# Performance work log

Hardware: AMD Instinct MI355X
Metric: run time of the kernel (lower is better)

The kernel has to match this reference:

```python
import jax, jax.numpy as jnp
import numpy as np

D_MODEL = 1024
N_HEADS = 16
D_HEAD = D_MODEL // N_HEADS
RANK = 128
KNOW_RANK = 128
N_COMPRESS = 64
N_EXPAND = 32
N_KNOW = 16384
TOPK_C = 8
TOPK_E = 4
KNOW_K = 8
B, S = 8, 1024
EPS_LN = 1e-5


def setup_inputs() -> dict:
    key = jax.random.key(0)
    ks = jax.random.split(key, 16)
    inp = {
        'x': jax.random.normal(ks[0], (B, S, D_MODEL), jnp.float32),
        'importance': jax.random.uniform(ks[1], (B, S), jnp.float32),
        # routers, stored as [d_model, n] so out = x @ W
        'Wc': jax.random.normal(ks[2], (D_MODEL, N_COMPRESS), jnp.float32) * 0.02,
        'WQr': jax.random.normal(ks[3], (D_MODEL, N_EXPAND), jnp.float32) * 0.02,
        'WKr': jax.random.normal(ks[4], (D_MODEL, N_EXPAND), jnp.float32) * 0.02,
        'WVr': jax.random.normal(ks[5], (D_MODEL, N_EXPAND), jnp.float32) * 0.02,
        'Wm': jax.random.normal(ks[6], (D_MODEL, N_COMPRESS), jnp.float32) * 0.02,
        # shared neuron pools
        'compress_neurons': jax.random.normal(ks[7], (N_COMPRESS, D_MODEL, RANK), jnp.float32) / np.sqrt(D_MODEL),
        'expand_pool': jax.random.normal(ks[8], (N_EXPAND, RANK, D_MODEL), jnp.float32) / np.sqrt(RANK),
        'knowledge_K': jax.random.normal(ks[9], (N_KNOW, KNOW_RANK), jnp.float32) * 0.02,
        'knowledge_V': jax.random.normal(ks[10], (N_KNOW, D_MODEL), jnp.float32) * 0.02,
        # output projection stored as [d_in, d_out]
        'W_O': jax.random.normal(ks[11], (D_MODEL, D_MODEL), jnp.float32) / np.sqrt(D_MODEL),
        'ln1_s': jnp.ones((D_MODEL,), jnp.float32),
        'ln1_b': jnp.zeros((D_MODEL,), jnp.float32),
        'ln2_s': jnp.ones((D_MODEL,), jnp.float32),
        'ln2_b': jnp.zeros((D_MODEL,), jnp.float32),
    }
    return inp


def _layernorm(x, s, b):
    mu = jnp.mean(x, axis=-1, keepdims=True)
    var = jnp.mean(jnp.square(x - mu), axis=-1, keepdims=True)
    return (x - mu) * jax.lax.rsqrt(var + EPS_LN) * s + b


def _topk_sparsify(w, k):
    # w: [B, n] -> sparse renormalized weights [B, n]
    vals, idx = jax.lax.top_k(w, k)
    rows = jnp.arange(w.shape[0])[:, None]
    sparse = jnp.zeros_like(w).at[rows, idx].set(vals)
    return sparse / (jnp.sum(sparse, axis=-1, keepdims=True) + 1e-8)


def _route(nx, importance, W, k):
    pref = jax.nn.softmax(jnp.einsum('bsd,dn->bsn', nx, W), axis=-1)
    dense = jnp.einsum('bs,bsn->bn', importance, pref)
    return _topk_sparsify(dense, k)


def _forward(x, importance, Wc, WQr, WKr, WVr, Wm, compress_neurons,
             expand_pool, knowledge_K, knowledge_V, W_O, ln1_s, ln1_b, ln2_s, ln2_b):
    Bx, Sx, D = x.shape
    n1 = _layernorm(x, ln1_s, ln1_b)

    # --- attention routing ---
    cw = _route(n1, importance, Wc, TOPK_C)
    ewQ = _route(n1, importance, WQr, TOPK_E)
    ewK = _route(n1, importance, WKr, TOPK_E)
    ewV = _route(n1, importance, WVr, TOPK_E)

    # --- synthesized low-rank attention weights ---
    shared_compress = jnp.einsum('bn,ndr->bdr', cw, compress_neurons)
    h = jnp.einsum('bsd,bdr->bsr', n1, shared_compress)
    EQ = jnp.einsum('bn,nrd->brd', ewQ, expand_pool)
    EK = jnp.einsum('bn,nrd->brd', ewK, expand_pool)
    EV = jnp.einsum('bn,nrd->brd', ewV, expand_pool)
    Q = jnp.einsum('bsr,brd->bsd', h, EQ).reshape(Bx, Sx, N_HEADS, D_HEAD).transpose(0, 2, 1, 3)
    K = jnp.einsum('bsr,brd->bsd', h, EK).reshape(Bx, Sx, N_HEADS, D_HEAD).transpose(0, 2, 1, 3)
    V = jnp.einsum('bsr,brd->bsd', h, EV).reshape(Bx, Sx, N_HEADS, D_HEAD).transpose(0, 2, 1, 3)

    scores = jnp.einsum('bhqd,bhkd->bhqk', Q, K) / np.sqrt(D_HEAD)
    causal = jnp.tril(jnp.ones((Sx, Sx), bool))
    scores = jnp.where(causal, scores, jnp.finfo(scores.dtype).min)
    attn = jax.nn.softmax(scores, axis=-1)
    attn_out = jnp.einsum('bhqk,bhkd->bhqd', attn, V).transpose(0, 2, 1, 3).reshape(Bx, Sx, D)
    attn_out = attn_out @ W_O
    x = x + attn_out

    # --- memory ---
    n2 = _layernorm(x, ln2_s, ln2_b)
    mw = _route(n2, importance, Wm, TOPK_C)
    sc_m = jnp.einsum('bn,ndr->bdr', mw, compress_neurons)
    Qm = jnp.einsum('bsd,bdr->bsr', n2, sc_m)  # knowledge_rank == rank -> no query_proj
    mscores = jnp.einsum('bsr,nr->bsn', Qm, knowledge_K) / np.sqrt(KNOW_RANK)
    topv, topi = jax.lax.top_k(mscores, KNOW_K)
    w = jax.nn.softmax(topv, axis=-1)  # [B,S,k]
    selV = knowledge_V[topi]  # [B,S,k,D]
    mem_out = jnp.einsum('bsk,bskd->bsd', w, selV)
    return x + mem_out


def reference(x, importance, Wc, WQr, WKr, WVr, Wm, compress_neurons,
              expand_pool, knowledge_K, knowledge_V, W_O, ln1_s, ln1_b, ln2_s, ln2_b):
    return _forward(x, importance, Wc, WQr, WKr, WVr, Wm, compress_neurons,
                    expand_pool, knowledge_K, knowledge_V, W_O, ln1_s, ln1_b, ln2_s, ln2_b)
```

## Files before the change

### kernel.cpp

```cpp
#include <hip/hip_runtime.h>
#include <hip/hip_bf16.h>

#define BD 8
#define SD 1024
#define DM 1024
#define NH 16
#define DH 64
#define RK 128
#define NK 16384

typedef __attribute__((ext_vector_type(8))) short bf16x8;
typedef __attribute__((ext_vector_type(4))) float f32x4;

__device__ __forceinline__ unsigned short f2b(float f) {
    unsigned u = __float_as_uint(f);
    unsigned r = (u + 0x7FFFu + ((u >> 16) & 1u)) >> 16;
    return (unsigned short)r;
}
__device__ __forceinline__ float b2f(unsigned short h) {
    return __uint_as_float(((unsigned)h) << 16);
}

__global__ void __launch_bounds__(256) ln_kernel(const float* __restrict__ x,
                                                 const float* __restrict__ sc,
                                                 const float* __restrict__ bi,
                                                 unsigned short* __restrict__ outh,
                                                 unsigned short* __restrict__ outl) {
    const int tok = blockIdx.x;
    __shared__ float xs[DM];
    __shared__ float red[256];
    const float* xp = x + (size_t)tok * DM;
    float s = 0.f;
    for (int i = threadIdx.x; i < DM; i += 256) { float v = xp[i]; xs[i] = v; s += v; }
    red[threadIdx.x] = s; __syncthreads();
    for (int st = 128; st; st >>= 1) { if (threadIdx.x < st) red[threadIdx.x] += red[threadIdx.x + st]; __syncthreads(); }
    float mu = red[0] * (1.f / DM);
    __syncthreads();
    float vs = 0.f;
    for (int i = threadIdx.x; i < DM; i += 256) { float d = xs[i] - mu; vs += d * d; }
    red[threadIdx.x] = vs; __syncthreads();
    for (int st = 128; st; st >>= 1) { if (threadIdx.x < st) red[threadIdx.x] += red[threadIdx.x + st]; __syncthreads(); }
    float rs = rsqrtf(red[0] * (1.f / DM) + 1e-5f);
    for (int i = threadIdx.x; i < DM; i += 256) {
        float v = (xs[i] - mu) * rs * sc[i] + bi[i];
        unsigned short h = f2b(v);
        outh[(size_t)tok * DM + i] = h;
        outl[(size_t)tok * DM + i] = f2b(v - b2f(h));
    }
}

__global__ void __launch_bounds__(256) prep_kernel(const float* __restrict__ Wc,
                                                   const float* __restrict__ WQr,
                                                   const float* __restrict__ WKr,
                                                   const float* __restrict__ WVr,
                                                   const float* __restrict__ Wm,
                                                   unsigned short* __restrict__ WTh,
                                                   unsigned short* __restrict__ WTl,
                                                   const float* __restrict__ WO,
                                                   unsigned short* __restrict__ WOt,
                                                   const float* __restrict__ kK,
                                                   unsigned short* __restrict__ kKb) {
    __shared__ float ls[64][65];
    const int t = threadIdx.x;
    const int bid = blockIdx.x;
    if (bid < 1024) {
        const int i = bid * 256 + t;
        const int c = i >> 10, d = i & 1023;
        float v = 0.f;
        if (c < 64)       v = Wc[d * 64 + c];
        else if (c < 96)  v = WQr[d * 32 + c - 64];
        else if (c < 128) v = WKr[d * 32 + c - 96];
        else if (c < 160) v = WVr[d * 32 + c - 128];
        else if (c >= 192) v = Wm[d * 64 + c - 192];
        unsigned short h = f2b(v);
        WTh[i] = h;
        WTl[i] = f2b(v - b2f(h));
    } else if (bid < 1280) {
        const int bz = bid - 1024;
        const int r0 = (bz >> 4) * 64, c0 = (bz & 15) * 64;
        #pragma unroll
        for (int p = 0; p < 16; p++) {
            const int e = p * 256 + t;
            const int r = e >> 6, c = e & 63;
            ls[r][c] = WO[(size_t)(r0 + r) * DM + c0 + c];
        }
        __syncthreads();
        #pragma unroll
        for (int p = 0; p < 16; p++) {
            const int e = p * 256 + t;
            const int c = e >> 6, r = e & 63;
            WOt[(size_t)(c0 + c) * DM + r0 + r] = f2b(ls[r][c]);
        }
    } else {
        const int i = (bid - 1280) * 256 + t;
        const float scale = 0.0883883476483184f;
        float4 v = ((const float4*)kK)[i];
        unsigned r0 = (unsigned)f2b(v.x * scale) | ((unsigned)f2b(v.y * scale) << 16);
        unsigned r1 = (unsigned)f2b(v.z * scale) | ((unsigned)f2b(v.w * scale) << 16);
        uint2 o; o.x = r0; o.y = r1;
        ((uint2*)kKb)[i] = o;
    }
}

__global__ void __launch_bounds__(256) gemm_split(const unsigned short* __restrict__ Ah,
                                                  const unsigned short* __restrict__ Al,
                                                  const unsigned short* __restrict__ Bh,
                                                  const unsigned short* __restrict__ Bl,
                                                  float* __restrict__ C,
                                                  int N, int K) {
    const int row0 = blockIdx.y * 64, col0 = blockIdx.x * 64;
    const int t = threadIdx.x;
    const int w = t >> 6, l = t & 63, lq = l & 15, lg = l >> 4;
    __shared__ unsigned short sAh[64 * 64];
    __shared__ unsigned short sAl[64 * 64];
    __shared__ unsigned short sBh[64 * 64];
    __shared__ unsigned short sBl[64 * 64];
    f32x4 acc[4];
    #pragma unroll
    for (int ni = 0; ni < 4; ni++) acc[ni] = f32x4{0.f, 0.f, 0.f, 0.f};

    for (int k0 = 0; k0 < K; k0 += 64) {
        __syncthreads();
        #pragma unroll
        for (int p = 0; p < 2; p++) {
            const int e = t * 8 + p * 2048;
            const int row = e >> 6, col = e & 63;
            const int sw = (e * 2) ^ ((row & 7) << 4);
            *(bf16x8*)((char*)sAh + sw) = *(const bf16x8*)(Ah + (size_t)(row0 + row) * K + k0 + col);
            *(bf16x8*)((char*)sAl + sw) = *(const bf16x8*)(Al + (size_t)(row0 + row) * K + k0 + col);
            *(bf16x8*)((char*)sBh + sw) = *(const bf16x8*)(Bh + (size_t)(col0 + row) * K + k0 + col);
            *(bf16x8*)((char*)sBl + sw) = *(const bf16x8*)(Bl + (size_t)(col0 + row) * K + k0 + col);
        }
        __syncthreads();
        #pragma unroll
        for (int kk = 0; kk < 2; kk++) {
            bf16x8 ah, al, bh[4], bl[4];
            {
                const int r = w * 16 + lq;
                const int off = (r * 128 + lg * 16 + kk * 64) ^ ((r & 7) << 4);
                ah = *(const bf16x8*)((const char*)sAh + off);
                al = *(const bf16x8*)((const char*)sAl + off);
            }
            #pragma unroll
            for (int ni = 0; ni < 4; ni++) {
                const int r = ni * 16 + lq;
                const int off = (r * 128 + lg * 16 + kk * 64) ^ ((r & 7) << 4);
                bh[ni] = *(const bf16x8*)((const char*)sBh + off);
                bl[ni] = *(const bf16x8*)((const char*)sBl + off);
            }
            #pragma unroll
            for (int ni = 0; ni < 4; ni++) {
                acc[ni] = __builtin_amdgcn_mfma_f32_16x16x32_bf16(ah, bh[ni], acc[ni], 0, 0, 0);
                acc[ni] = __builtin_amdgcn_mfma_f32_16x16x32_bf16(ah, bl[ni], acc[ni], 0, 0, 0);
                acc[ni] = __builtin_amdgcn_mfma_f32_16x16x32_bf16(al, bh[ni], acc[ni], 0, 0, 0);
            }
        }
    }
    #pragma unroll
    for (int j = 0; j < 4; j++) {
        const int row = row0 + w * 16 + lg * 4 + j;
        #pragma unroll
        for (int ni = 0; ni < 4; ni++)
            C[(size_t)row * N + col0 + ni * 16 + lq] = acc[ni][j];
    }
}

__global__ void __launch_bounds__(256) gemm_split_sm2(const unsigned short* __restrict__ Ah,
                                                      const unsigned short* __restrict__ Al,
                                                      const unsigned short* __restrict__ Bh,
                                                      const unsigned short* __restrict__ Bl,
                                                      const float* __restrict__ imp,
                                                      float* __restrict__ partial) {
    const int row0 = blockIdx.x * 64;
    const int K = DM;
    const int t = threadIdx.x;
    const int w = t >> 6, l = t & 63, lq = l & 15, lg = l >> 4;
    __shared__ unsigned short sAh[64 * 64];
    __shared__ unsigned short sAl[64 * 64];
    __shared__ unsigned short sBh[64 * 64];
    __shared__ unsigned short sBl[64 * 64];
    __shared__ float wsm[64][65];
    f32x4 acc[4];
    #pragma unroll
    for (int ni = 0; ni < 4; ni++) acc[ni] = f32x4{0.f, 0.f, 0.f, 0.f};

    for (int k0 = 0; k0 < K; k0 += 64) {
        __syncthreads();
        #pragma unroll
        for (int p = 0; p < 2; p++) {
            const int e = t * 8 + p * 2048;
            const int row = e >> 6, col = e & 63;
            const int sw = (e * 2) ^ ((row & 7) << 4);
            *(bf16x8*)((char*)sAh + sw) = *(const bf16x8*)(Ah + (size_t)(row0 + row) * K + k0 + col);
            *(bf16x8*)((char*)sAl + sw) = *(const bf16x8*)(Al + (size_t)(row0 + row) * K + k0 + col);
            *(bf16x8*)((char*)sBh + sw) = *(const bf16x8*)(Bh + (size_t)(row) * K + k0 + col);
            *(bf16x8*)((char*)sBl + sw) = *(const bf16x8*)(Bl + (size_t)(row) * K + k0 + col);
        }
        __syncthreads();
        #pragma unroll
        for (int kk = 0; kk < 2; kk++) {
            bf16x8 ah, al, bh[4], bl[4];
            {
                const int r = w * 16 + lq;
                const int off = (r * 128 + lg * 16 + kk * 64) ^ ((r & 7) << 4);
                ah = *(const bf16x8*)((const char*)sAh + off);
                al = *(const bf16x8*)((const char*)sAl + off);
            }
            #pragma unroll
            for (int ni = 0; ni < 4; ni++) {
                const int r = ni * 16 + lq;
                const int off = (r * 128 + lg * 16 + kk * 64) ^ ((r & 7) << 4);
                bh[ni] = *(const bf16x8*)((const char*)sBh + off);
                bl[ni] = *(const bf16x8*)((const char*)sBl + off);
            }
            #pragma unroll
            for (int ni = 0; ni < 4; ni++) {
                acc[ni] = __builtin_amdgcn_mfma_f32_16x16x32_bf16(ah, bh[ni], acc[ni], 0, 0, 0);
                acc[ni] = __builtin_amdgcn_mfma_f32_16x16x32_bf16(ah, bl[ni], acc[ni], 0, 0, 0);
                acc[ni] = __builtin_amdgcn_mfma_f32_16x16x32_bf16(al, bh[ni], acc[ni], 0, 0, 0);
            }
        }
    }
    #pragma unroll
    for (int j = 0; j < 4; j++) {
        float mx = fmaxf(fmaxf(acc[0][j], acc[1][j]), fmaxf(acc[2][j], acc[3][j]));
        #pragma unroll
        for (int d = 1; d < 16; d <<= 1) mx = fmaxf(mx, __shfl_xor(mx, d));
        float e0 = __expf(acc[0][j] - mx), e1 = __expf(acc[1][j] - mx);
        float e2 = __expf(acc[2][j] - mx), e3 = __expf(acc[3][j] - mx);
        float ss = e0 + e1 + e2 + e3;
        #pragma unroll
        for (int d = 1; d < 16; d <<= 1) ss += __shfl_xor(ss, d);
        const int rl = w * 16 + lg * 4 + j;
        const float scl = imp[row0 + rl] / ss;
        wsm[rl][lq]      = e0 * scl;
        wsm[rl][16 + lq] = e1 * scl;
        wsm[rl][32 + lq] = e2 * scl;
        wsm[rl][48 + lq] = e3 * scl;
    }
    __syncthreads();
    if (t < 64) {
        float s = 0.f;
        for (int k = 0; k < 64; k++) s += wsm[k][t];
        const int b = row0 >> 10, chunk = (row0 >> 6) & 15;
        partial[((size_t)(b * 16 + chunk)) * 224 + 160 + t] = s;
    }
}

__global__ void __launch_bounds__(256) softpref_red(const float* __restrict__ lgt,
                                                    const float* __restrict__ imp,
                                                    float* __restrict__ partial) {
    const int b = blockIdx.x, chunk = blockIdx.y;
    __shared__ float wp[64][161];
    const int t = threadIdx.x;
    const int tl = t >> 2, sg = t & 3;
    const int tok = b * SD + chunk * 64 + tl;
    const int o = (sg == 0) ? 0 : (64 + 32 * (sg - 1));
    const int n = (sg == 0) ? 64 : 32;
    const float* lp = lgt + (size_t)tok * 192 + o;
    float m = -1e30f;
    for (int i = 0; i < n; i++) m = fmaxf(m, lp[i]);
    float ss = 0.f;
    for (int i = 0; i < n; i++) ss += __expf(lp[i] - m);
    const float scl = imp[tok] / ss;
    for (int i = 0; i < n; i++) wp[tl][o + i] = __expf(lp[i] - m) * scl;
    __syncthreads();
    if (t < 160) {
        float s = 0.f;
        for (int k = 0; k < 64; k++) s += wp[k][t];
        partial[((size_t)(b * 16 + chunk)) * 224 + t] = s;
    }
}

__global__ void topk_kernel(const float* __restrict__ partial,
                            int* __restrict__ ridx, float* __restrict__ rw,
                            int r0, int nr) {
    __shared__ float dv[40][65];
    const int t = threadIdx.x;
    if (t >= BD * nr) return;
    const int b = t / nr, r = r0 + (t % nr);
    const int offs[5] = {0, 64, 96, 128, 160};
    const int ns[5]   = {64, 32, 32, 32, 64};
    const int ks[5]   = {8, 4, 4, 4, 8};
    const int n = ns[r], k = ks[r], off = offs[r];
    for (int i = 0; i < n; i++) {
        float s = 0.f;
        for (int c = 0; c < 16; c++) s += partial[((size_t)(b * 16 + c)) * 224 + off + i];
        dv[t][i] = s;
    }
    unsigned long long mask = 0;
    float vals[8]; int idxs[8];
    float ssum = 0.f;
    for (int kk = 0; kk < k; kk++) {
        float best = -1e30f; int bi = 0;
        for (int i = 0; i < n; i++)
            if (!((mask >> i) & 1ull) && dv[t][i] > best) { best = dv[t][i]; bi = i; }
        mask |= 1ull << bi;
        vals[kk] = best; idxs[kk] = bi; ssum += best;
    }
    float inv = 1.f / (ssum + 1e-8f);
    for (int kk = 0; kk < 8; kk++) {
        ridx[(b * 5 + r) * 8 + kk] = (kk < k) ? idxs[kk] : 0;
        rw[(b * 5 + r) * 8 + kk]   = (kk < k) ? vals[kk] * inv : 0.f;
    }
}

__global__ void __launch_bounds__(256) combine_all_kernel(const float* __restrict__ cneu,
                                                          const float* __restrict__ epool,
                                                          const int* __restrict__ ridx,
                                                          const float* __restrict__ rw,
                                                          unsigned short* __restrict__ scompT,
                                                          unsigned short* __restrict__ E3t) {
    __shared__ float ls[64][65];
    const int t = threadIdx.x;
    const int bid = blockIdx.x;
    const float* pool;
    int b, router, r0, c0, Rp, Cp;
    unsigned short* op;
    if (bid < 256) {
        b = bid >> 5;
        const int rem = bid & 31;
        c0 = (rem & 1) * 64; r0 = (rem >> 1) * 64;
        Rp = DM; Cp = RK; router = 0; pool = cneu;
        op = scompT + (size_t)b * DM * RK;
    } else {
        const int e = bid - 256;
        const int z = e >> 5;
        const int rem = e & 31;
        c0 = (rem & 15) * 64; r0 = (rem >> 4) * 64;
        b = z & 7; router = 1 + (z >> 3);
        Rp = RK; Cp = DM; pool = epool;
        op = E3t + (size_t)b * 3 * DM * RK + (size_t)(router - 1) * DM * RK;
    }
    const int* ii = ridx + (b * 5 + router) * 8;
    const float* ww = rw + (b * 5 + router) * 8;
    const int kc = (router == 0) ? 8 : 4;
    const int rr = t >> 4, cc = (t & 15) * 4;
    #pragma unroll
    for (int p = 0; p < 4; p++) {
        const int r = rr + p * 16;
        float4 acc = {0.f, 0.f, 0.f, 0.f};
        for (int kk = 0; kk < kc; kk++) {
            const float w = ww[kk];
            float4 v = *(const float4*)&pool[((size_t)ii[kk] * Rp + r0 + r) * Cp + c0 + cc];
            acc.x += w * v.x; acc.y += w * v.y; acc.z += w * v.z; acc.w += w * v.w;
        }
        ls[r][cc] = acc.x; ls[r][cc + 1] = acc.y; ls[r][cc + 2] = acc.z; ls[r][cc + 3] = acc.w;
    }
    __syncthreads();
    #pragma unroll
    for (int q = 0; q < 2; q++) {
        const int c = (t >> 3) + q * 32;
        const int r8 = (t & 7) * 8;
        union { unsigned short s[8]; bf16x8 v; } u;
        #pragma unroll
        for (int j = 0; j < 8; j++) u.s[j] = f2b(ls[r8 + j][c]);
        *(bf16x8*)(op + (size_t)(c0 + c) * Rp + r0 + r8) = u.v;
    }
}

__global__ void __launch_bounds__(256) combine_t_kernel(const float* __restrict__ pool,
                                                        const int* __restrict__ ridx,
                                                        const float* __restrict__ rw,
                                                        int router, int kc,
                                                        unsigned short* __restrict__ outT,
                                                        int Rp, int Cp, long long sOut) {
    const int b = blockIdx.z;
    const int r0 = blockIdx.y * 64, c0 = blockIdx.x * 64;
    __shared__ float ls[64][65];
    const int* ii = ridx + (b * 5 + router) * 8;
    const float* ww = rw + (b * 5 + router) * 8;
    const int t = threadIdx.x;
    const int rr = t >> 4, cc = (t & 15) * 4;
    #pragma unroll
    for (int p = 0; p < 4; p++) {
        const int r = rr + p * 16;
        float4 acc = {0.f, 0.f, 0.f, 0.f};
        for (int kk = 0; kk < kc; kk++) {
            const float w = ww[kk];
            float4 v = *(const float4*)&pool[((size_t)ii[kk] * Rp + r0 + r) * Cp + c0 + cc];
            acc.x += w * v.x; acc.y += w * v.y; acc.z += w * v.z; acc.w += w * v.w;
        }
        ls[r][cc] = acc.x; ls[r][cc + 1] = acc.y; ls[r][cc + 2] = acc.z; ls[r][cc + 3] = acc.w;
    }
    __syncthreads();
    unsigned short* op = outT + (size_t)b * sOut;
    #pragma unroll
    for (int q = 0; q < 2; q++) {
        const int c = (t >> 3) + q * 32;
        const int r8 = (t & 7) * 8;
        union { unsigned short s[8]; bf16x8 v; } u;
        #pragma unroll
        for (int j = 0; j < 8; j++) u.s[j] = f2b(ls[r8 + j][c]);
        *(bf16x8*)(op + (size_t)(c0 + c) * Rp + r0 + r8) = u.v;
    }
}

template<int OUTB, int HASX>
__global__ void __launch_bounds__(256) gemm_bf16(const unsigned short* __restrict__ A,
                                                 const unsigned short* __restrict__ Bt,
                                                 const float* __restrict__ X,
                                                 void* __restrict__ Cv,
                                                 int M, int N, int K,
                                                 long long sA, long long sB, long long sC) {
    const int bz = blockIdx.z;
    const unsigned short* Ab = A + (size_t)bz * sA;
    const unsigned short* Btb = Bt + (size_t)bz * sB;
    const int row0 = blockIdx.y * 128, col0 = blockIdx.x * 128;
    const int t = threadIdx.x;
    const int w = t >> 6, l = t & 63, lq = l & 15, lg = l >> 4;
    const int wr = w >> 1, wc = w & 1;
    __shared__ unsigned short As[128 * 64];
    __shared__ unsigned short Bs[128 * 64];
    f32x4 acc[4][4];
    #pragma unroll
    for (int mi = 0; mi < 4; mi++)
        #pragma unroll
        for (int ni = 0; ni < 4; ni++) acc[mi][ni] = f32x4{0.f, 0.f, 0.f, 0.f};

    for (int k0 = 0; k0 < K; k0 += 64) {
        __syncthreads();
        #pragma unroll
        for (int p = 0; p < 4; p++) {
            const int e = t * 8 + p * 2048;
            const int row = e >> 6, col = e & 63;
            bf16x8 va = *(const bf16x8*)(Ab + (size_t)(row0 + row) * K + k0 + col);
            *(bf16x8*)((char*)As + ((row * 128 + col * 2) ^ ((row & 7) << 4))) = va;
            bf16x8 vb = *(const bf16x8*)(Btb + (size_t)(col0 + row) * K + k0 + col);
            *(bf16x8*)((char*)Bs + ((row * 128 + col * 2) ^ ((row & 7) << 4))) = vb;
        }
        __syncthreads();
        #pragma unroll
        for (int kk = 0; kk < 2; kk++) {
            bf16x8 af[4], bg[4];
            #pragma unroll
            for (int mi = 0; mi < 4; mi++) {
                const int r = wr * 64 + mi * 16 + lq;
                af[mi] = *(const bf16x8*)((const char*)As + ((r * 128 + lg * 16 + kk * 64) ^ ((r & 7) << 4)));
            }
            #pragma unroll
            for (int ni = 0; ni < 4; ni++) {
                const int r = wc * 64 + ni * 16 + lq;
                bg[ni] = *(const bf16x8*)((const char*)Bs + ((r * 128 + lg * 16 + kk * 64) ^ ((r & 7) << 4)));
            }
            #pragma unroll
            for (int mi = 0; mi < 4; mi++)
                #pragma unroll
                for (int ni = 0; ni < 4; ni++)
                    acc[mi][ni] = __builtin_amdgcn_mfma_f32_16x16x32_bf16(af[mi], bg[ni], acc[mi][ni], 0, 0, 0);
        }
    }
    #pragma unroll
    for (int mi = 0; mi < 4; mi++) {
        #pragma unroll
        for (int j = 0; j < 4; j++) {
            const int row = row0 + wr * 64 + mi * 16 + lg * 4 + j;
            #pragma unroll
            for (int ni = 0; ni < 4; ni++) {
                const int col = col0 + wc * 64 + ni * 16 + lq;
                float v = acc[mi][ni][j];
                if (HASX) v += X[(size_t)row * N + col];
                if (OUTB) ((unsigned short*)Cv)[(size_t)bz * sC + (size_t)row * N + col] = f2b(v);
                else      ((float*)Cv)[(size_t)bz * sC + (size_t)row * N + col] = v;
            }
        }
    }
}

__global__ void __launch_bounds__(256) gemm_h(const unsigned short* __restrict__ A,
                                              const unsigned short* __restrict__ Bt,
                                              unsigned short* __restrict__ C,
                                              int K,
                                              long long sA, long long sB, long long sC) {
    const int bz = blockIdx.z;
    const unsigned short* Ab = A + (size_t)bz * sA;
    const unsigned short* Btb = Bt + (size_t)bz * sB;
    const int row0 = blockIdx.y * 64;
    const int t = threadIdx.x;
    const int w = t >> 6, l = t & 63, lq = l & 15, lg = l >> 4;
    __shared__ unsigned short As[64 * 64];
    __shared__ unsigned short Bs[128 * 64];
    f32x4 acc[8];
    #pragma unroll
    for (int ni = 0; ni < 8; ni++) acc[ni] = f32x4{0.f, 0.f, 0.f, 0.f};

    for (int k0 = 0; k0 < K; k0 += 64) {
        __syncthreads();
        #pragma unroll
        for (int p = 0; p < 2; p++) {
            const int e = t * 8 + p * 2048;
            const int row = e >> 6, col = e & 63;
            bf16x8 va = *(const bf16x8*)(Ab + (size_t)(row0 + row) * K + k0 + col);
            *(bf16x8*)((char*)As + ((row * 128 + col * 2) ^ ((row & 7) << 4))) = va;
        }
        #pragma unroll
        for (int p = 0; p < 4; p++) {
            const int e = t * 8 + p * 2048;
            const int row = e >> 6, col = e & 63;
            bf16x8 vb = *(const bf16x8*)(Btb + (size_t)row * K + k0 + col);
            *(bf16x8*)((char*)Bs + ((row * 128 + col * 2) ^ ((row & 7) << 4))) = vb;
        }
        __syncthreads();
        #pragma unroll
        for (int kk = 0; kk < 2; kk++) {
            const int ra = w * 16 + lq;
            bf16x8 af = *(const bf16x8*)((const char*)As + ((ra * 128 + lg * 16 + kk * 64) ^ ((ra & 7) << 4)));
            #pragma unroll
            for (int ni = 0; ni < 8; ni++) {
                const int r = ni * 16 + lq;
                bf16x8 bg = *(const bf16x8*)((const char*)Bs + ((r * 128 + lg * 16 + kk * 64) ^ ((r & 7) << 4)));
                acc[ni] = __builtin_amdgcn_mfma_f32_16x16x32_bf16(af, bg, acc[ni], 0, 0, 0);
            }
        }
    }
    #pragma unroll
    for (int j = 0; j < 4; j++) {
        const int row = row0 + w * 16 + lg * 4 + j;
        #pragma unroll
        for (int ni = 0; ni < 8; ni++)
            C[(size_t)bz * sC + (size_t)row * 128 + ni * 16 + lq] = f2b(acc[ni][j]);
    }
}

#define SWZV(d) (((((d) >> 1) ^ ((d) >> 3)) & 7) << 4)
__global__ void __launch_bounds__(256) attn_mfma_kernel(const unsigned short* __restrict__ Q,
                                                        const unsigned short* __restrict__ K,
                                                        const unsigned short* __restrict__ V,
                                                        unsigned short* __restrict__ O,
                                                        int ldq) {
    const int qt = blockIdx.x, hh = blockIdx.y, b = blockIdx.z;
    const int t = threadIdx.x;
    const int w = t >> 6, l = t & 63, lq = l & 15, lg = l >> 4;

    __shared__ unsigned short ks[2][64 * 64];
    __shared__ unsigned short vt[2][64 * 64];
    __shared__ unsigned short pl[4][16 * 64];

    const size_t base = (size_t)b * SD * ldq + (size_t)hh * DH;
    const size_t obase = (size_t)b * SD * DM + (size_t)hh * DH;
    const int qA = qt;
    const int qB = 15 - qt;

    bf16x8 aqA[2], aqB[2];
    {
        const unsigned short* qp = Q + base + (size_t)(qA * 64 + w * 16 + lq) * ldq + lg * 8;
        aqA[0] = *(const bf16x8*)qp; aqA[1] = *(const bf16x8*)(qp + 32);
        const unsigned short* qp2 = Q + base + (size_t)(qB * 64 + w * 16 + lq) * ldq + lg * 8;
        aqB[0] = *(const bf16x8*)qp2; aqB[1] = *(const bf16x8*)(qp2 + 32);
    }

    f32x4 oA[4], oB[4];
    #pragma unroll
    for (int dt = 0; dt < 4; dt++) { oA[dt] = f32x4{0.f,0.f,0.f,0.f}; oB[dt] = f32x4{0.f,0.f,0.f,0.f}; }
    float mA[4] = {-1e30f,-1e30f,-1e30f,-1e30f}, sA[4] = {0.f,0.f,0.f,0.f};
    float mB[4] = {-1e30f,-1e30f,-1e30f,-1e30f}, sB[4] = {0.f,0.f,0.f,0.f};

    const int ntile = 16 - qt;
    const int srow = t >> 3;
    const int scol = (t & 7) * 8;

    int cur = 0;

    #pragma unroll
    for (int p = 0; p < 2; p++) {
        const int row = srow + 32 * p;
        bf16x8 kv = *(const bf16x8*)(K + base + (size_t)row * ldq + scol);
        *(bf16x8*)((char*)&ks[0][0] + ((row * 128 + scol * 2) ^ ((row & 7) << 4))) = kv;
        bf16x8 vv = *(const bf16x8*)(V + base + (size_t)row * ldq + scol);
        #pragma unroll
        for (int j2 = 0; j2 < 8; j2++) {
            const int d = scol + j2;
            *(unsigned short*)((char*)&vt[0][0] + ((d * 128 + row * 2) ^ SWZV(d))) = (unsigned short)vv[j2];
        }
    }
    __syncthreads();

    auto compute = [&](int q0, const bf16x8* aq, f32x4* o_, float* m_, float* s_, int kt) {
        const f32x4 zero4 = {0.f, 0.f, 0.f, 0.f};
        f32x4 sacc[4];
        __builtin_amdgcn_s_setprio(1);
        #pragma unroll
        for (int ct = 0; ct < 4; ct++) {
            const int krow = ct * 16 + lq;
            bf16x8 b0 = *(const bf16x8*)((const char*)&ks[cur][0] + ((krow * 128 + lg * 16) ^ ((lq & 7) << 4)));
            bf16x8 b1 = *(const bf16x8*)((const char*)&ks[cur][0] + ((krow * 128 + lg * 16 + 64) ^ ((lq & 7) << 4)));
            f32x4 s = __builtin_amdgcn_mfma_f32_16x16x32_bf16(aq[0], b0, zero4, 0, 0, 0);
            s = __builtin_amdgcn_mfma_f32_16x16x32_bf16(aq[1], b1, s, 0, 0, 0);
            sacc[ct] = s;
        }
        __builtin_amdgcn_s_setprio(0);
        float tm[4];
        #pragma unroll
        for (int j = 0; j < 4; j++) {
            const int qg = q0 * 64 + w * 16 + lg * 4 + j;
            float mx = -1e30f;
            #pragma unroll
            for (int ct = 0; ct < 4; ct++) {
                const int kg = kt * 64 + ct * 16 + lq;
                float v = sacc[ct][j] * 0.125f;
                v = (kg <= qg) ? v : -1e30f;
                sacc[ct][j] = v;
                mx = fmaxf(mx, v);
            }
            #pragma unroll
            for (int d = 1; d < 16; d <<= 1) mx = fmaxf(mx, __shfl_xor(mx, d));
            tm[j] = mx;
        }
        #pragma unroll
        for (int j = 0; j < 4; j++) {
            const float nm = fmaxf(m_[j], tm[j]);
            const float so = __expf(m_[j] - nm);
            m_[j] = nm;
            float rs = 0.f;
            const int prow = lg * 4 + j;
            #pragma unroll
            for (int ct = 0; ct < 4; ct++) {
                const float p = __expf(sacc[ct][j] - nm);
                rs += p;
                const int byteoff = ((prow * 128) + (ct * 16 + lq) * 2) ^ ((prow & 7) << 4);
                *(unsigned short*)((char*)&pl[w][0] + byteoff) = f2b(p);
            }
            #pragma unroll
            for (int d = 1; d < 16; d <<= 1) rs += __shfl_xor(rs, d);
            s_[j] = s_[j] * so + rs;
            #pragma unroll
            for (int dt = 0; dt < 4; dt++) o_[dt][j] *= so;
        }
        asm volatile("s_waitcnt lgkmcnt(0)" ::: "memory");
        __builtin_amdgcn_sched_barrier(0);
        __builtin_amdgcn_s_setprio(1);
        #pragma unroll
        for (int c = 0; c < 2; c++) {
            bf16x8 pa = *(const bf16x8*)((const char*)&pl[w][0] +
                          ((lq * 128 + lg * 16 + 64 * c) ^ ((lq & 7) << 4)));
            #pragma unroll
            for (int dt = 0; dt < 4; dt++) {
                const int dd = dt * 16 + lq;
                bf16x8 bv = *(const bf16x8*)((const char*)&vt[cur][0] +
                              ((dd * 128 + lg * 16 + 64 * c) ^ SWZV(dd)));
                o_[dt] = __builtin_amdgcn_mfma_f32_16x16x32_bf16(pa, bv, o_[dt], 0, 0, 0);
            }
        }
        __builtin_amdgcn_s_setprio(0);
    };

    const int mymaxA = qA * 64 + w * 16 + 15;
    for (int kt = 0; kt < ntile; kt++) {
        bf16x8 kN[2], vN[2];
        const bool pre = (kt + 1 < ntile);
        if (pre) {
            #pragma unroll
            for (int p = 0; p < 2; p++) {
                const int row = srow + 32 * p;
                kN[p] = *(const bf16x8*)(K + base + (size_t)((kt + 1) * 64 + row) * ldq + scol);
                vN[p] = *(const bf16x8*)(V + base + (size_t)((kt + 1) * 64 + row) * ldq + scol);
            }
        }
        compute(qB, aqB, oB, mB, sB, kt);
        if (kt * 64 <= mymaxA) compute(qA, aqA, oA, mA, sA, kt);
        if (pre) {
            #pragma unroll
            for (int p = 0; p < 2; p++) {
                const int row = srow + 32 * p;
                *(bf16x8*)((char*)&ks[cur ^ 1][0] + ((row * 128 + scol * 2) ^ ((row & 7) << 4))) = kN[p];
                #pragma unroll
                for (int j2 = 0; j2 < 8; j2++) {
                    const int d = scol + j2;
                    *(unsigned short*)((char*)&vt[cur ^ 1][0] + ((d * 128 + row * 2) ^ SWZV(d))) =
                        (unsigned short)vN[p][j2];
                }
            }
        }
        __syncthreads();
        cur ^= 1;
    }

    #pragma unroll
    for (int j = 0; j < 4; j++) {
        const float invA = 1.f / sA[j];
        const float invB = 1.f / sB[j];
        const int rowA = qA * 64 + w * 16 + lg * 4 + j;
        const int rowB = qB * 64 + w * 16 + lg * 4 + j;
        unsigned short* opA = O + obase + (size_t)rowA * DM;
        unsigned short* opB = O + obase + (size_t)rowB * DM;
        #pragma unroll
        for (int dt = 0; dt < 4; dt++) {
            opA[dt * 16 + lq] = f2b(oA[dt][j] * invA);
            opB[dt * 16 + lq] = f2b(oB[dt][j] * invB);
        }
    }
}
#undef SWZV

#define CE(a, b) { float hi_ = fmaxf(a, b), lo_ = fminf(a, b); a = hi_; b = lo_; }
__global__ void __launch_bounds__(512, 2) know_kernel(const unsigned short* __restrict__ Qmb,
                                                      const unsigned short* __restrict__ kKb,
                                                      const float* __restrict__ kV,
                                                      float* __restrict__ out) {
    const int t = threadIdx.x;
    const int w = t >> 6, l = t & 63, lq = l & 15, lg = l >> 4;
    const int tok0 = blockIdx.x * 32;
    __shared__ unsigned short ks[8][16 * 128];
    __shared__ float cs[32][64];

    bf16x8 aq[2][4];
    #pragma unroll
    for (int g = 0; g < 2; g++) {
        const unsigned short* qp = Qmb + (size_t)(tok0 + g * 16 + lq) * 128 + lg * 8;
        #pragma unroll
        for (int c = 0; c < 4; c++) aq[g][c] = *(const bf16x8*)(qp + c * 32);
    }

    float L[2][4][8];
    #pragma unroll
    for (int g = 0; g < 2; g++)
        #pragma unroll
        for (int j = 0; j < 4; j++)
            #pragma unroll
            for (int s = 0; s < 8; s++) L[g][j][s] = __uint_as_float(0xF2000000u | (unsigned)s);

    const unsigned short* gsrc = kKb + (((size_t)w * 2048) << 7) + l * 8;
    unsigned short* myks = &ks[w][0];

    bf16x8 vreg[4];
    #pragma unroll
    for (int p = 0; p < 4; p++) vreg[p] = *(const bf16x8*)(gsrc + p * 512);

    for (int t4 = 0; t4 < 32; t4++) {
        float B[2][4][4];
        #pragma unroll
        for (int sub = 0; sub < 4; sub++) {
            const int kt = t4 * 4 + sub;
            #pragma unroll
            for (int p = 0; p < 4; p++) {
                const int e = p * 512 + l * 8;
                const int row = e >> 7;
                *(bf16x8*)((char*)myks + ((e * 2) ^ ((row & 7) << 4))) = vreg[p];
            }
            if (kt < 127) {
                const unsigned short* src2 = gsrc + (size_t)(kt + 1) * 2048;
                #pragma unroll
                for (int p = 0; p < 4; p++) vreg[p] = *(const bf16x8*)(src2 + p * 512);
            }
            {
                const char* kb = (const char*)myks + lq * 256;
                const int sw = (lq & 7) << 4;
                f32x4 s0 = {0.f, 0.f, 0.f, 0.f};
                f32x4 s1 = {0.f, 0.f, 0.f, 0.f};
                #pragma unroll
                for (int c = 0; c < 4; c++) {
                    bf16x8 bv = *(const bf16x8*)(kb + ((c * 64 + lg * 16) ^ sw));
                    s0 = __builtin_amdgcn_mfma_f32_16x16x32_bf16(aq[0][c], bv, s0, 0, 0, 0);
                    s1 = __builtin_amdgcn_mfma_f32_16x16x32_bf16(aq[1][c], bv, s1, 0, 0, 0);
                }
                const unsigned keyb = (unsigned)(w * 2048 + kt * 16 + lq);
                #pragma unroll
                for (int j = 0; j < 4; j++) {
                    B[0][j][sub] = __uint_as_float((__float_as_uint(s0[j]) & 0xFFFFC000u) | keyb);
                    B[1][j][sub] = __uint_as_float((__float_as_uint(s1[j]) & 0xFFFFC000u) | keyb);
                }
            }
        }
        #pragma unroll
        for (int g = 0; g < 2; g++)
            #pragma unroll
            for (int j = 0; j < 4; j++) {
                const float bmax = fmaxf(fmaxf(B[g][j][0], B[g][j][1]), fmaxf(B[g][j][2], B[g][j][3]));
                if (__any(bmax > L[g][j][7])) {
                    CE(B[g][j][0], B[g][j][2]); CE(B[g][j][1], B[g][j][3]);
                    CE(B[g][j][0], B[g][j][1]); CE(B[g][j][2], B[g][j][3]);
                    CE(B[g][j][1], B[g][j][2]);
                    L[g][j][4] = fmaxf(L[g][j][4], B[g][j][3]);
                    L[g][j][5] = fmaxf(L[g][j][5], B[g][j][2]);
                    L[g][j][6] = fmaxf(L[g][j][6], B[g][j][1]);
                    L[g][j][7] = fmaxf(L[g][j][7], B[g][j][0]);
                    CE(L[g][j][0], L[g][j][4]); CE(L[g][j][1], L[g][j][5]); CE(L[g][j][2], L[g][j][6]); CE(L[g][j][3], L[g][j][7]);
                    CE(L[g][j][0], L[g][j][2]); CE(L[g][j][1], L[g][j][3]); CE(L[g][j][4], L[g][j][6]); CE(L[g][j][5], L[g][j][7]);
                    CE(L[g][j][0], L[g][j][1]); CE(L[g][j][2], L[g][j][3]); CE(L[g][j][4], L[g][j][5]); CE(L[g][j][6], L[g][j][7]);
                }
            }
    }
    #pragma unroll
    for (int g = 0; g < 2; g++)
        #pragma unroll
        for (int j = 0; j < 4; j++) {
            #pragma unroll
            for (int d = 1; d < 16; d <<= 1) {
                float P[8];
                #pragma unroll
                for (int s = 0; s < 8; s++) P[s] = __shfl_xor(L[g][j][s], d);
                L[g][j][0] = fmaxf(L[g][j][0], P[7]);
                L[g][j][1] = fmaxf(L[g][j][1], P[6]);
                L[g][j][2] = fmaxf(L[g][j][2], P[5]);
                L[g][j][3] = fmaxf(L[g][j][3], P[4]);
                L[g][j][4] = fmaxf(L[g][j][4], P[3]);
                L[g][j][5] = fmaxf(L[g][j][5], P[2]);
                L[g][j][6] = fmaxf(L[g][j][6], P[1]);
                L[g][j][7] = fmaxf(L[g][j][7], P[0]);
                CE(L[g][j][0], L[g][j][4]); CE(L[g][j][1], L[g][j][5]); CE(L[g][j][2], L[g][j][6]); CE(L[g][j][3], L[g][j][7]);
                CE(L[g][j][0], L[g][j][2]); CE(L[g][j][1], L[g][j][3]); CE(L[g][j][4], L[g][j][6]); CE(L[g][j][5], L[g][j][7]);
                CE(L[g][j][0], L[g][j][1]); CE(L[g][j][2], L[g][j][3]); CE(L[g][j][4], L[g][j][5]); CE(L[g][j][6], L[g][j][7]);
            }
        }
    if (lq == 0) {
        #pragma unroll
        for (int g = 0; g < 2; g++)
            #pragma unroll
            for (int j = 0; j < 4; j++) {
                const int tl = g * 16 + lg * 4 + j;
                #pragma unroll
                for (int ss = 0; ss < 8; ss++) cs[tl][w * 8 + ss] = L[g][j][ss];
            }
    }
    __syncthreads();

    #pragma unroll
    for (int ti = 0; ti < 4; ti++) {
        const int tl = w * 4 + ti;
        float lv = cs[tl][l];
        float topv[8]; int topi[8];
        #pragma unroll
        for (int kk = 0; kk < 8; kk++) {
            float m = lv;
            #pragma unroll
            for (int d = 1; d < 64; d <<= 1) m = fmaxf(m, __shfl_xor(m, d));
            topv[kk] = m;
            topi[kk] = (int)(__float_as_uint(m) & 0x3FFFu);
            lv = (lv == m) ? -1e31f : lv;
        }
        const float mx = topv[0];
        float e[8]; float ssum = 0.f;
        #pragma unroll
        for (int kk = 0; kk < 8; kk++) { e[kk] = __expf(topv[kk] - mx); ssum += e[kk]; }
        const float inv = 1.f / ssum;

        float4 acc[4];
        #pragma unroll
        for (int ch = 0; ch < 4; ch++) acc[ch] = float4{0.f, 0.f, 0.f, 0.f};
        #pragma unroll
        for (int kk = 0; kk < 8; kk++) {
            const float wk = e[kk] * inv;
            const float* vp = kV + ((size_t)topi[kk] << 10);
            #pragma unroll
            for (int ch = 0; ch < 4; ch++) {
                float4 v = *(const float4*)(vp + ch * 256 + l * 4);
                acc[ch].x += wk * v.x; acc[ch].y += wk * v.y;
                acc[ch].z += wk * v.z; acc[ch].w += wk * v.w;
            }
        }
        float* op = out + ((size_t)(tok0 + tl) << 10);
        #pragma unroll
        for (int ch = 0; ch < 4; ch++) {
            float4 o = *(const float4*)(op + ch * 256 + l * 4);
            o.x += acc[ch].x; o.y += acc[ch].y; o.z += acc[ch].z; o.w += acc[ch].w;
            *(float4*)(op + ch * 256 + l * 4) = o;
        }
    }
}
#undef CE

extern "C" void kernel_launch(void* const* d_in, const int* in_sizes, int n_in,
                              void* d_out, int out_size, void* d_ws, size_t ws_size,
                              hipStream_t stream) {
    const float* x    = (const float*)d_in[0];
    const float* imp  = (const float*)d_in[1];
    const float* Wc   = (const float*)d_in[2];
    const float* WQr  = (const float*)d_in[3];
    const float* WKr  = (const float*)d_in[4];
    const float* WVr  = (const float*)d_in[5];
    const float* Wm   = (const float*)d_in[6];
    const float* cneu = (const float*)d_in[7];
    const float* epool= (const float*)d_in[8];
    const float* kK   = (const float*)d_in[9];
    const float* kV   = (const float*)d_in[10];
    const float* WO   = (const float*)d_in[11];
    const float* ln1s = (const float*)d_in[12];
    const float* ln1b = (const float*)d_in[13];
    const float* ln2s = (const float*)d_in[14];
    const float* ln2b = (const float*)d_in[15];
    float* out = (float*)d_out;

    float* ws = (float*)d_ws;
    size_t o = 0;
    unsigned short* n1h = (unsigned short*)(ws + o); o += (size_t)BD * SD * DM / 2;
    unsigned short* n1l = (unsigned short*)(ws + o); o += (size_t)BD * SD * DM / 2;
    float* lgt   = ws + o; o += (size_t)BD * SD * 192;
    float* partial = ws + o; o += (size_t)BD * 16 * 224;
    int*   ridx  = (int*)(ws + o); o += (size_t)BD * 5 * 8;
    float* rw    = ws + o; o += (size_t)BD * 5 * 8;
    unsigned short* WTh = (unsigned short*)(ws + o); o += (size_t)256 * 1024 / 2;
    unsigned short* WTl = (unsigned short*)(ws + o); o += (size_t)256 * 1024 / 2;
    unsigned short* scompT = (unsigned short*)(ws + o); o += (size_t)BD * RK * DM / 2;
    unsigned short* E3t = (unsigned short*)(ws + o); o += (size_t)BD * 3 * DM * RK / 2;
    unsigned short* hb  = (unsigned short*)(ws + o); o += (size_t)BD * SD * RK / 2;
    unsigned short* QKV16 = (unsigned short*)(ws + o); o += (size_t)BD * SD * 3072 / 2;
    unsigned short* attnb = (unsigned short*)(ws + o); o += (size_t)BD * SD * DM / 2;
    unsigned short* WOt = (unsigned short*)(ws + o); o += (size_t)DM * DM / 2;
    unsigned short* kKb = (unsigned short*)(ws + o); o += (size_t)NK * RK / 2;
    unsigned short* Qmb = (unsigned short*)(ws + o); o += (size_t)BD * SD * RK / 2;

    const int NTOK = BD * SD;
    const long long sE3 = (long long)3 * DM * RK;

    prep_kernel<<<3328, 256, 0, stream>>>(Wc, WQr, WKr, WVr, Wm, WTh, WTl, WO, WOt, kK, kKb);

    ln_kernel<<<NTOK, 256, 0, stream>>>(x, ln1s, ln1b, n1h, n1l);
    gemm_split<<<dim3(3, NTOK / 64), 256, 0, stream>>>(n1h, n1l, WTh, WTl, lgt, 192, DM);
    softpref_red<<<dim3(BD, 16), 256, 0, stream>>>(lgt, imp, partial);
    topk_kernel<<<1, 64, 0, stream>>>(partial, ridx, rw, 0, 4);
    combine_all_kernel<<<1024, 256, 0, stream>>>(cneu, epool, ridx, rw, scompT, E3t);
    gemm_h<<<dim3(1, SD / 64, BD), 256, 0, stream>>>(n1h, scompT, hb,
        DM, (long long)SD * DM, (long long)RK * DM, (long long)SD * RK);
    gemm_bf16<1, 0><<<dim3(24, 8, BD), 256, 0, stream>>>(hb, E3t, nullptr, QKV16,
        SD, 3072, RK, (long long)SD * RK, sE3, (long long)SD * 3072);
    attn_mfma_kernel<<<dim3(8, NH, BD), 256, 0, stream>>>(QKV16, QKV16 + 1024, QKV16 + 2048,
        attnb, 3072);
    gemm_bf16<0, 1><<<dim3(8, 64, 1), 256, 0, stream>>>(attnb, WOt, x, out,
        NTOK, DM, DM, 0, 0, 0);

    ln_kernel<<<NTOK, 256, 0, stream>>>(out, ln2s, ln2b, n1h, n1l);
    gemm_split_sm2<<<NTOK / 64, 256, 0, stream>>>(n1h, n1l,
        WTh + (size_t)192 * 1024, WTl + (size_t)192 * 1024, imp, partial);
    topk_kernel<<<1, 64, 0, stream>>>(partial, ridx, rw, 4, 1);
    combine_t_kernel<<<dim3(2, 16, BD), 256, 0, stream>>>(cneu, ridx, rw, 4, 8, scompT, DM, RK,
        (long long)DM * RK);
    gemm_h<<<dim3(1, SD / 64, BD), 256, 0, stream>>>(n1h, scompT, Qmb,
        DM, (long long)SD * DM, (long long)RK * DM, (long long)SD * RK);
    know_kernel<<<NTOK / 32, 512, 0, stream>>>(Qmb, kKb, kV, out);
}
```

Before: 573.6 us.

## Split knowledge top-k scoring across two key halves with separate merge kernel

The knowledge scoring kernel now handles half of the 16384 keys per block, giving twice as many blocks (256 to 512). Each block writes its per-token top-8 candidates to a workspace buffer. A new merge kernel picks the final top-8 from the 16 candidates, then does the softmax and value gather. The aim is more parallelism and shorter per-block serial loops, at the cost of an extra launch and a small candidate round-trip through memory.

```diff
diff --git a/kernel.cpp b/kernel.cpp
--- a/kernel.cpp
+++ b/kernel.cpp
@@ -693,13 +693,13 @@
 #undef SWZV
 
 #define CE(a, b) { float hi_ = fmaxf(a, b), lo_ = fminf(a, b); a = hi_; b = lo_; }
-__global__ void __launch_bounds__(512, 2) know_kernel(const unsigned short* __restrict__ Qmb,
-                                                      const unsigned short* __restrict__ kKb,
-                                                      const float* __restrict__ kV,
-                                                      float* __restrict__ out) {
+__global__ void __launch_bounds__(512, 2) know_score(const unsigned short* __restrict__ Qmb,
+                                                     const unsigned short* __restrict__ kKb,
+                                                     float* __restrict__ cand) {
     const int t = threadIdx.x;
     const int w = t >> 6, l = t & 63, lq = l & 15, lg = l >> 4;
     const int tok0 = blockIdx.x * 32;
+    const int half = blockIdx.y;
     __shared__ unsigned short ks[8][16 * 128];
     __shared__ float cs[32][64];
 
@@ -719,14 +719,15 @@
             #pragma unroll
             for (int s = 0; s < 8; s++) L[g][j][s] = __uint_as_float(0xF2000000u | (unsigned)s);
 
-    const unsigned short* gsrc = kKb + (((size_t)w * 2048) << 7) + l * 8;
+    const int kbase = half * 8192 + w * 1024;
+    const unsigned short* gsrc = kKb + (((size_t)kbase) << 7) + l * 8;
     unsigned short* myks = &ks[w][0];
 
     bf16x8 vreg[4];
     #pragma unroll
     for (int p = 0; p < 4; p++) vreg[p] = *(const bf16x8*)(gsrc + p * 512);
 
-    for (int t4 = 0; t4 < 32; t4++) {
+    for (int t4 = 0; t4 < 16; t4++) {
         float B[2][4][4];
         #pragma unroll
         for (int sub = 0; sub < 4; sub++) {
@@ -737,7 +738,7 @@
                 const int row = e >> 7;
                 *(bf16x8*)((char*)myks + ((e * 2) ^ ((row & 7) << 4))) = vreg[p];
             }
-            if (kt < 127) {
+            if (kt < 63) {
                 const unsigned short* src2 = gsrc + (size_t)(kt + 1) * 2048;
                 #pragma unroll
                 for (int p = 0; p < 4; p++) vreg[p] = *(const bf16x8*)(src2 + p * 512);
@@ -753,7 +754,7 @@
                     s0 = __builtin_amdgcn_mfma_f32_16x16x32_bf16(aq[0][c], bv, s0, 0, 0, 0);
                     s1 = __builtin_amdgcn_mfma_f32_16x16x32_bf16(aq[1][c], bv, s1, 0, 0, 0);
                 }
-                const unsigned keyb = (unsigned)(w * 2048 + kt * 16 + lq);
+                const unsigned keyb = (unsigned)(kbase + kt * 16 + lq);
                 #pragma unroll
                 for (int j = 0; j < 4; j++) {
                     B[0][j][sub] = __uint_as_float((__float_as_uint(s0[j]) & 0xFFFFC000u) | keyb);
@@ -818,6 +819,28 @@
     for (int ti = 0; ti < 4; ti++) {
         const int tl = w * 4 + ti;
         float lv = cs[tl][l];
+        float* cp = cand + ((size_t)(tok0 + tl) * 2 + half) * 8;
+        #pragma unroll
+        for (int kk = 0; kk < 8; kk++) {
+            float m = lv;
+            #pragma unroll
+            for (int d = 1; d < 64; d <<= 1) m = fmaxf(m, __shfl_xor(m, d));
+            if (l == 0) cp[kk] = m;
+            lv = (lv == m) ? -1e31f : lv;
+        }
+    }
+}
+#undef CE
+
+__global__ void __launch_bounds__(256) know_merge(const float* __restrict__ cand,
+                                                  const float* __restrict__ kV,
+                                                  float* __restrict__ out) {
+    const int t = threadIdx.x;
+    const int w = t >> 6, l = t & 63;
+    #pragma unroll
+    for (int ti = 0; ti < 2; ti++) {
+        const int tok = blockIdx.x * 8 + w * 2 + ti;
+        float lv = (l < 16) ? cand[(size_t)tok * 16 + l] : -1e31f;
         float topv[8]; int topi[8];
         #pragma unroll
         for (int kk = 0; kk < 8; kk++) {
@@ -848,7 +871,7 @@
                 acc[ch].z += wk * v.z; acc[ch].w += wk * v.w;
             }
         }
-        float* op = out + ((size_t)(tok0 + tl) << 10);
+        float* op = out + ((size_t)tok << 10);
         #pragma unroll
         for (int ch = 0; ch < 4; ch++) {
             float4 o = *(const float4*)(op + ch * 256 + l * 4);
@@ -857,7 +880,6 @@
         }
     }
 }
-#undef CE
 
 extern "C" void kernel_launch(void* const* d_in, const int* in_sizes, int n_in,
                               void* d_out, int out_size, void* d_ws, size_t ws_size,
@@ -898,6 +920,7 @@
     unsigned short* WOt = (unsigned short*)(ws + o); o += (size_t)DM * DM / 2;
     unsigned short* kKb = (unsigned short*)(ws + o); o += (size_t)NK * RK / 2;
     unsigned short* Qmb = (unsigned short*)(ws + o); o += (size_t)BD * SD * RK / 2;
+    float* cand = ws + o; o += (size_t)BD * SD * 16;
 
     const int NTOK = BD * SD;
     const long long sE3 = (long long)3 * DM * RK;
@@ -926,5 +949,6 @@
         (long long)DM * RK);
     gemm_h<<<dim3(1, SD / 64, BD), 256, 0, stream>>>(n1h, scompT, Qmb,
         DM, (long long)SD * DM, (long long)RK * DM, (long long)SD * RK);
-    know_kernel<<<NTOK / 32, 512, 0, stream>>>(Qmb, kKb, kV, out);
-}
+    know_score<<<dim3(NTOK / 32, 2), 512, 0, stream>>>(Qmb, kKb, cand);
+    know_merge<<<NTOK / 8, 256, 0, stream>>>(cand, kV, out);
+}
```

Measured after the change: 598.9 us. 1.04x slower.

## Pre-swizzle knowledge keys into MFMA fragment layout and load directly to registers

Applied to the files above, without the earlier changes.

The preprocessing kernel now writes the bf16 knowledge_K matrix in a layout that matches the per-lane MFMA B-fragment order. The knowledge scoring kernel then loads each 16-key tile straight from global memory into registers, double-buffered, with no LDS staging. This removes the LDS writes and reads and frees LDS per block, which may help occupancy. The cost is that keys are read from global or L2 without a shared-memory copy, so the loop depends more on load latency.

```diff
diff --git a/kernel.cpp b/kernel.cpp
--- a/kernel.cpp
+++ b/kernel.cpp
@@ -98,7 +98,12 @@
         unsigned r0 = (unsigned)f2b(v.x * scale) | ((unsigned)f2b(v.y * scale) << 16);
         unsigned r1 = (unsigned)f2b(v.z * scale) | ((unsigned)f2b(v.w * scale) << 16);
         uint2 o; o.x = r0; o.y = r1;
-        ((uint2*)kKb)[i] = o;
+        const int k = i >> 5;
+        const int d = (i & 31) * 4;
+        const int kt = k >> 4, lq = k & 15;
+        const int c = d >> 5, lg2 = (d >> 3) & 3, o8 = d & 7;
+        const size_t idx = (size_t)kt * 2048 + c * 512 + lg2 * 128 + lq * 8 + o8;
+        *(uint2*)(kKb + idx) = o;
     }
 }
 
@@ -700,7 +705,6 @@
     const int t = threadIdx.x;
     const int w = t >> 6, l = t & 63, lq = l & 15, lg = l >> 4;
     const int tok0 = blockIdx.x * 32;
-    __shared__ unsigned short ks[8][16 * 128];
     __shared__ float cs[32][64];
 
     bf16x8 aq[2][4];
@@ -719,39 +723,31 @@
             #pragma unroll
             for (int s = 0; s < 8; s++) L[g][j][s] = __uint_as_float(0xF2000000u | (unsigned)s);
 
-    const unsigned short* gsrc = kKb + (((size_t)w * 2048) << 7) + l * 8;
-    unsigned short* myks = &ks[w][0];
-
-    bf16x8 vreg[4];
-    #pragma unroll
-    for (int p = 0; p < 4; p++) vreg[p] = *(const bf16x8*)(gsrc + p * 512);
+    const unsigned short* kb = kKb + ((size_t)(w * 128) * 2048) + l * 8;
+
+    bf16x8 vA[4], vB[4];
+    #pragma unroll
+    for (int c = 0; c < 4; c++) vA[c] = *(const bf16x8*)(kb + c * 512);
 
     for (int t4 = 0; t4 < 32; t4++) {
         float B[2][4][4];
         #pragma unroll
         for (int sub = 0; sub < 4; sub++) {
             const int kt = t4 * 4 + sub;
-            #pragma unroll
-            for (int p = 0; p < 4; p++) {
-                const int e = p * 512 + l * 8;
-                const int row = e >> 7;
-                *(bf16x8*)((char*)myks + ((e * 2) ^ ((row & 7) << 4))) = vreg[p];
-            }
+            const bf16x8* curv = (sub & 1) ? vB : vA;
+            bf16x8* nxtv = (sub & 1) ? vA : vB;
             if (kt < 127) {
-                const unsigned short* src2 = gsrc + (size_t)(kt + 1) * 2048;
+                const unsigned short* src2 = kb + (size_t)(kt + 1) * 2048;
                 #pragma unroll
-                for (int p = 0; p < 4; p++) vreg[p] = *(const bf16x8*)(src2 + p * 512);
+                for (int p = 0; p < 4; p++) nxtv[p] = *(const bf16x8*)(src2 + p * 512);
             }
             {
-                const char* kb = (const char*)myks + lq * 256;
-                const int sw = (lq & 7) << 4;
                 f32x4 s0 = {0.f, 0.f, 0.f, 0.f};
                 f32x4 s1 = {0.f, 0.f, 0.f, 0.f};
                 #pragma unroll
                 for (int c = 0; c < 4; c++) {
-                    bf16x8 bv = *(const bf16x8*)(kb + ((c * 64 + lg * 16) ^ sw));
-                    s0 = __builtin_amdgcn_mfma_f32_16x16x32_bf16(aq[0][c], bv, s0, 0, 0, 0);
-                    s1 = __builtin_amdgcn_mfma_f32_16x16x32_bf16(aq[1][c], bv, s1, 0, 0, 0);
+                    s0 = __builtin_amdgcn_mfma_f32_16x16x32_bf16(aq[0][c], curv[c], s0, 0, 0, 0);
+                    s1 = __builtin_amdgcn_mfma_f32_16x16x32_bf16(aq[1][c], curv[c], s1, 0, 0, 0);
                 }
                 const unsigned keyb = (unsigned)(w * 2048 + kt * 16 + lq);
                 #pragma unroll
```

Result: no change. 576.7 us (+0.5%).
